# Performance work log

Hardware: AMD Instinct MI355X
Metric: run time of the kernel (lower is better)

The kernel has to match this reference:

```python
import jax, jax.numpy as jnp
import numpy as np

N_NODES = 100000
N_EDGES = 1600000
D_IN = 128
D_OUT = 128
EPSILON = 0.0


def setup_inputs() -> dict:
    key = jax.random.key(0)
    k1, k2, k3, k4, k5 = jax.random.split(key, 5)
    indices = jax.random.randint(k1, (2, N_EDGES), 0, N_NODES, dtype=jnp.int64 if jax.config.jax_enable_x64 else jnp.int32)
    values = jax.random.uniform(k2, (N_EDGES,), dtype=jnp.float32)
    features = jax.random.normal(k3, (N_NODES, D_IN), dtype=jnp.float32)
    # Xavier-uniform linear weights, zero biases (as in init_parameters)
    lim1 = float(np.sqrt(6.0 / (D_IN + D_OUT)))
    lim2 = float(np.sqrt(6.0 / (D_OUT + D_OUT)))
    W1 = jax.random.uniform(k4, (D_IN, D_OUT), minval=-lim1, maxval=lim1, dtype=jnp.float32)
    W2 = jax.random.uniform(k5, (D_OUT, D_OUT), minval=-lim2, maxval=lim2, dtype=jnp.float32)
    b1 = jnp.zeros((D_OUT,), dtype=jnp.float32)
    b2 = jnp.zeros((D_OUT,), dtype=jnp.float32)
    return {"indices": indices, "values": values, "features": features,
            "W1": W1, "b1": b1, "W2": W2, "b2": b2}


def reference(indices, values, features, W1, b1, W2, b2):
    row, col = indices[0], indices[1]
    # SpMM: out[r] = sum_e values[e] * features[col[e]]  (sparse_adj @ features)
    messages = values[:, None] * features[col]              # [E, D_IN]
    neighbor = jax.ops.segment_sum(messages, row, num_segments=N_NODES)  # [N, D_IN]
    combined = (1.0 + EPSILON) * features + neighbor        # epsilon residual
    h = jax.nn.relu(combined @ W1 + b1)                     # Linear -> ReLU
    out = h @ W2 + b2                                       # Linear
    # dropout is identity in eval mode
    return out
```

## Files before the change

kernel.cpp:

```cpp
#include <hip/hip_runtime.h>

#define N_NODES 100000
#define N_EDGES 1600000
#define D 128
#define CB 98
#define CCAP 17920

typedef unsigned short u16;
typedef unsigned int u32;
typedef __attribute__((ext_vector_type(8))) short bf16x8;
typedef __attribute__((ext_vector_type(4))) float f32x4;

__device__ __forceinline__ u16 f2bf(float f) {
    u32 u = __float_as_uint(f);
    u += 0x7fffu + ((u >> 16) & 1u);
    return (u16)(u >> 16);
}


#define BIN_BLKS 391

__global__ __launch_bounds__(256) void prep_bin(
    const int* __restrict__ row, const int* __restrict__ col,
    const float* __restrict__ val,
    int* __restrict__ coarseCount, int2* __restrict__ binned) {
    __shared__ int h[CB];
    __shared__ int lb[CB];
    int bid = blockIdx.x;
    int t = threadIdx.x;

    if (t < CB) h[t] = 0;
    __syncthreads();
    int base = bid * 4096;
    int r[16];
#pragma unroll
    for (int i = 0; i < 16; ++i) {
        int e = base + i * 256 + t;
        r[i] = (e < N_EDGES) ? row[e] : -1;
        if (r[i] >= 0) atomicAdd(&h[r[i] >> 10], 1);
    }
    __syncthreads();
    if (t < CB) {
        int c = h[t];
        lb[t] = c ? atomicAdd(&coarseCount[t * 16], c) : 0;
        h[t] = 0;
    }
    __syncthreads();
#pragma unroll
    for (int i = 0; i < 16; ++i) {
        if (r[i] < 0) continue;
        int e = base + i * 256 + t;
        int cb = r[i] >> 10;
        int pos = cb * CCAP + lb[cb] + atomicAdd(&h[cb], 1);
        int2 ev;
        ev.x = col[e] | ((r[i] & 1023) << 17);
        ev.y = __float_as_int(val[e]);
        binned[pos] = ev;
    }
}


#define SORT_BLKS 98
#define CVF_BLKS 1563
#define CVW_BLKS 32

__global__ __launch_bounds__(1024) void sortk_conv(
    const int2* __restrict__ binned, const int* __restrict__ coarseCount,
    int2* __restrict__ rowRange, int2* __restrict__ scev,
    const float* __restrict__ features, u32* __restrict__ featb,
    const float* __restrict__ W1, const float* __restrict__ W2,
    u16* __restrict__ W1t, u16* __restrict__ W2t) {
    __shared__ int h[1024];
    __shared__ int cur[1024];
    __shared__ int wsum[16];
    __shared__ int wbase[16];
    int b = blockIdx.x, t = threadIdx.x;

    if (b >= SORT_BLKS) {
        int cid = b - SORT_BLKS;
        if (cid < CVF_BLKS) {
            int idx = cid * 1024 + t;
            if (idx < N_NODES * D / 8) {
                const float4* f4 = (const float4*)features;
                float4 a = f4[idx * 2], bb = f4[idx * 2 + 1];
                uint4 o;
                o.x = (u32)f2bf(a.x) | ((u32)f2bf(a.y) << 16);
                o.y = (u32)f2bf(a.z) | ((u32)f2bf(a.w) << 16);
                o.z = (u32)f2bf(bb.x) | ((u32)f2bf(bb.y) << 16);
                o.w = (u32)f2bf(bb.z) | ((u32)f2bf(bb.w) << 16);
                ((uint4*)featb)[idx] = o;
            }
        } else {
            int flat = (cid - CVF_BLKS) * 1024 + t;
            int m = flat >> 14;
            int idx = flat & 16383;
            int n = idx & 127;
            int k = idx >> 7;
            const float* src = m ? W2 : W1;
            u16* dst = m ? W2t : W1t;
            dst[n * 128 + k] = f2bf(src[k * 128 + n]);
        }
        return;
    }

    int lane = t & 63, wv = t >> 6;
    int row0 = b << 10;
    int lo = b * CCAP;
    int cnt = coarseCount[b * 16];

    h[t] = 0;
    __syncthreads();
    for (int i = t; i < cnt; i += 1024)
        atomicAdd(&h[((u32)binned[lo + i].x) >> 17], 1);
    __syncthreads();

    int c = h[t];
    int x = c;
#pragma unroll
    for (int d = 1; d < 64; d <<= 1) {
        int y = __shfl_up(x, d);
        if (lane >= d) x += y;
    }
    if (lane == 63) wsum[wv] = x;
    __syncthreads();
    if (t < 16) {
        int s = wsum[t], sx = s;
#pragma unroll
        for (int d = 1; d < 16; d <<= 1) {
            int y = __shfl_up(sx, d);
            if (lane >= d) sx += y;
        }
        wbase[t] = sx - s;
    }
    __syncthreads();
    int start = lo + wbase[wv] + (x - c);
    if (row0 + t < N_NODES) rowRange[row0 + t] = make_int2(start, start + c);
    cur[t] = start;
    __syncthreads();

    for (int i = t; i < cnt; i += 1024) {
        int2 ev = binned[lo + i];
        int rl = ((u32)ev.x) >> 17;
        int pos = atomicAdd(&cur[rl], 1);
        scev[pos] = make_int2(ev.x & 0x1FFFF, ev.y);
    }
}


__global__ __launch_bounds__(256) void spmm_bf16(
    const int2* __restrict__ scev, const int2* __restrict__ rowRange,
    const u32* __restrict__ featb, u32* __restrict__ Xb) {
    int wid0 = (blockIdx.x * blockDim.x + threadIdx.x) >> 6;
    int wid = __builtin_amdgcn_readfirstlane(wid0);
    int lane = threadIdx.x & 63;
    if (wid >= N_NODES) return;
    int2 rr = rowRange[wid];
    int j = rr.x, end = rr.y;
    u32 self = featb[wid * 64 + lane];
    float ax0 = __uint_as_float(self << 16);
    float ay0 = __uint_as_float(self & 0xffff0000u);
    float ax1 = 0.f, ay1 = 0.f;
    for (; j < end; j += 16) {
        int2 e[16];
        u32 p[16];
#pragma unroll
        for (int u = 0; u < 16; ++u) {
            int idx = j + u;
            int c = (idx < end) ? idx : (end - 1);
            e[u] = scev[c];
            if (idx >= end) e[u].y = 0;
        }
#pragma unroll
        for (int u = 0; u < 16; ++u) p[u] = featb[e[u].x * 64 + lane];
#pragma unroll
        for (int u = 0; u < 16; ++u) {
            float v = __int_as_float(e[u].y);
            float lo = __uint_as_float(p[u] << 16);
            float hi = __uint_as_float(p[u] & 0xffff0000u);
            if (u & 1) {
                ax1 += v * lo;
                ay1 += v * hi;
            } else {
                ax0 += v * lo;
                ay0 += v * hi;
            }
        }
    }
    float accx = ax0 + ax1;
    float accy = ay0 + ay1;
    Xb[wid * 64 + lane] = (u32)f2bf(accx) | ((u32)f2bf(accy) << 16);
}


__global__ __launch_bounds__(256, 2) void gemm_fused(
    const u16* __restrict__ Xb, const u16* __restrict__ W1t,
    const float* __restrict__ b1, const u16* __restrict__ W2t,
    const float* __restrict__ b2, float* __restrict__ outf) {
    __shared__ u16 Ws[128][136];
    u16(*Ht)[130] = (u16(*)[130]) & Ws[0][0];

    int t = threadIdx.x;
    {
        const uint4* wsrc = (const uint4*)W1t;
#pragma unroll
        for (int i = 0; i < 8; ++i) {
            int f = t + 256 * i;
            *(uint4*)&Ws[f >> 4][(f & 15) << 3] = wsrc[f];
        }
    }
    __syncthreads();

    int w = t >> 6, lane = t & 63;
    int quad = lane >> 4, l16 = lane & 15;
    int row0 = blockIdx.x * 128 + w * 32;

    f32x4 acc[2][8];
#pragma unroll
    for (int rt = 0; rt < 2; ++rt)
#pragma unroll
        for (int ct = 0; ct < 8; ++ct) acc[rt][ct] = (f32x4){0.f, 0.f, 0.f, 0.f};

    int ra = row0 + l16;
    int rb = row0 + 16 + l16;
    if (ra > N_NODES - 1) ra = N_NODES - 1;
    if (rb > N_NODES - 1) rb = N_NODES - 1;
    const u16* pa = Xb + (size_t)ra * D + quad * 8;
    const u16* pb = Xb + (size_t)rb * D + quad * 8;

#pragma unroll
    for (int kb = 0; kb < 128; kb += 32) {
        bf16x8 a0 = *(const bf16x8*)(pa + kb);
        bf16x8 a1 = *(const bf16x8*)(pb + kb);
#pragma unroll
        for (int ct = 0; ct < 8; ++ct) {
            bf16x8 b = *(const bf16x8*)&Ws[ct * 16 + l16][kb + quad * 8];
            acc[0][ct] = __builtin_amdgcn_mfma_f32_16x16x32_bf16(a0, b, acc[0][ct], 0, 0, 0);
            acc[1][ct] = __builtin_amdgcn_mfma_f32_16x16x32_bf16(a1, b, acc[1][ct], 0, 0, 0);
        }
    }

    float bv1[8];
#pragma unroll
    for (int ct = 0; ct < 8; ++ct) bv1[ct] = b1[ct * 16 + l16];

    __syncthreads();

    int hbase = w * 32;
#pragma unroll
    for (int rt = 0; rt < 2; ++rt) {
#pragma unroll
        for (int ct = 0; ct < 8; ++ct) {
            float v0 = fmaxf(acc[rt][ct][0] + bv1[ct], 0.f);
            float v1 = fmaxf(acc[rt][ct][1] + bv1[ct], 0.f);
            float v2 = fmaxf(acc[rt][ct][2] + bv1[ct], 0.f);
            float v3 = fmaxf(acc[rt][ct][3] + bv1[ct], 0.f);
            u16* dst = &Ht[ct * 16 + l16][hbase + rt * 16 + quad * 4];
            ((u32*)dst)[0] = (u32)f2bf(v0) | ((u32)f2bf(v1) << 16);
            ((u32*)dst)[1] = (u32)f2bf(v2) | ((u32)f2bf(v3) << 16);
        }
    }
    __syncthreads();

    f32x4 acc2[2][8];
#pragma unroll
    for (int rt = 0; rt < 2; ++rt)
#pragma unroll
        for (int ct = 0; ct < 8; ++ct) acc2[rt][ct] = (f32x4){0.f, 0.f, 0.f, 0.f};

#pragma unroll
    for (int kb = 0; kb < 128; kb += 32) {
        bf16x8 a0, a1;
#pragma unroll
        for (int i = 0; i < 8; ++i) {
            a0[i] = (short)Ht[kb + quad * 8 + i][hbase + l16];
            a1[i] = (short)Ht[kb + quad * 8 + i][hbase + 16 + l16];
        }
#pragma unroll
        for (int ct = 0; ct < 8; ++ct) {
            bf16x8 b = *(const bf16x8*)(W2t + (size_t)(ct * 16 + l16) * D + kb + quad * 8);
            acc2[0][ct] = __builtin_amdgcn_mfma_f32_16x16x32_bf16(a0, b, acc2[0][ct], 0, 0, 0);
            acc2[1][ct] = __builtin_amdgcn_mfma_f32_16x16x32_bf16(a1, b, acc2[1][ct], 0, 0, 0);
        }
    }

    float bv2[8];
#pragma unroll
    for (int ct = 0; ct < 8; ++ct) bv2[ct] = b2[ct * 16 + l16];

#pragma unroll
    for (int rt = 0; rt < 2; ++rt) {
#pragma unroll
        for (int r = 0; r < 4; ++r) {
            int row = row0 + rt * 16 + quad * 4 + r;
            if (row >= N_NODES) continue;
#pragma unroll
            for (int ct = 0; ct < 8; ++ct) {
                outf[(size_t)row * D + ct * 16 + l16] = acc2[rt][ct][r] + bv2[ct];
            }
        }
    }
}

extern "C" void kernel_launch(void* const* d_in, const int* in_sizes, int n_in,
                              void* d_out, int out_size, void* d_ws, size_t ws_size,
                              hipStream_t stream) {
    const int* indices = (const int*)d_in[0];
    const float* values = (const float*)d_in[1];
    const float* features = (const float*)d_in[2];
    const float* W1 = (const float*)d_in[3];
    const float* b1 = (const float*)d_in[4];
    const float* W2 = (const float*)d_in[5];
    const float* b2 = (const float*)d_in[6];

    const int* row = indices;
    const int* col = indices + N_EDGES;

    int* wsI = (int*)d_ws;
    int* coarseCount = wsI;
    int2* rowRange = (int2*)(wsI + 1600);
    int2* scev = (int2*)(wsI + 1600 + 2 * N_NODES);
    u32* Xb = (u32*)(wsI + 1600 + 2 * N_NODES + 2 * CB * CCAP);
    u16* W1t = (u16*)(Xb + (size_t)N_NODES * 64);
    u16* W2t = W1t + 16384;

    int2* binned = (int2*)d_out;
    u32* featb = (u32*)((char*)d_out + (size_t)N_NODES * D * 2);
    float* outf = (float*)d_out;

    hipMemsetAsync(coarseCount, 0, CB * 16 * sizeof(int), stream);

    prep_bin<<<BIN_BLKS, 256, 0, stream>>>(row, col, values, coarseCount, binned);

    sortk_conv<<<SORT_BLKS + CVF_BLKS + CVW_BLKS, 1024, 0, stream>>>(
        binned, coarseCount, rowRange, scev, features, featb, W1, W2, W1t, W2t);

    spmm_bf16<<<(N_NODES * 64 + 255) / 256, 256, 0, stream>>>(scev, rowRange, featb, Xb);

    gemm_fused<<<(N_NODES + 127) / 128, 256, 0, stream>>>(
        (const u16*)Xb, W1t, b1, W2t, b2, outf);
}
```

Before: 254.4 us.

## Halve binning work per block, vectorize SpMM FMAs, raise GEMM occupancy hint

The binning kernel now handles 2048 edges per block instead of 4096 and loads col and val alongside row in the first pass, so they are held in registers and not re-read later. The SpMM accumulation switches to two-wide float vectors so the compiler can emit packed FMA instructions. The fused GEMM launch bound raises its minimum blocks per SM from 2 to 3, which pressures register allocation and risks spills. These are several unrelated tweaks across three kernels.

Result: no change. 254.1 us (-0.1%).

```diff
diff --git a/kernel.cpp b/kernel.cpp
--- a/kernel.cpp
+++ b/kernel.cpp
@@ -10,6 +10,7 @@
 typedef unsigned int u32;
 typedef __attribute__((ext_vector_type(8))) short bf16x8;
 typedef __attribute__((ext_vector_type(4))) float f32x4;
+typedef __attribute__((ext_vector_type(2))) float f32x2;
 
 __device__ __forceinline__ u16 f2bf(float f) {
     u32 u = __float_as_uint(f);
@@ -18,7 +19,7 @@
 }
 
 
-#define BIN_BLKS 391
+#define BIN_BLKS 782
 
 __global__ __launch_bounds__(256) void prep_bin(
     const int* __restrict__ row, const int* __restrict__ col,
@@ -31,30 +32,33 @@
 
     if (t < CB) h[t] = 0;
     __syncthreads();
-    int base = bid * 4096;
-    int r[16];
-#pragma unroll
-    for (int i = 0; i < 16; ++i) {
+    int base = bid * 2048;
+    int r[8], c[8];
+    float v[8];
+#pragma unroll
+    for (int i = 0; i < 8; ++i) {
         int e = base + i * 256 + t;
-        r[i] = (e < N_EDGES) ? row[e] : -1;
-        if (r[i] >= 0) atomicAdd(&h[r[i] >> 10], 1);
+        bool ok = (e < N_EDGES);
+        r[i] = ok ? row[e] : -1;
+        c[i] = ok ? col[e] : 0;
+        v[i] = ok ? val[e] : 0.f;
+        if (ok) atomicAdd(&h[r[i] >> 10], 1);
     }
     __syncthreads();
     if (t < CB) {
-        int c = h[t];
-        lb[t] = c ? atomicAdd(&coarseCount[t * 16], c) : 0;
+        int cc = h[t];
+        lb[t] = cc ? atomicAdd(&coarseCount[t * 16], cc) : 0;
         h[t] = 0;
     }
     __syncthreads();
 #pragma unroll
-    for (int i = 0; i < 16; ++i) {
+    for (int i = 0; i < 8; ++i) {
         if (r[i] < 0) continue;
-        int e = base + i * 256 + t;
         int cb = r[i] >> 10;
         int pos = cb * CCAP + lb[cb] + atomicAdd(&h[cb], 1);
         int2 ev;
-        ev.x = col[e] | ((r[i] & 1023) << 17);
-        ev.y = __float_as_int(val[e]);
+        ev.x = c[i] | ((r[i] & 1023) << 17);
+        ev.y = __float_as_int(v[i]);
         binned[pos] = ev;
     }
 }
@@ -157,9 +161,11 @@
     int2 rr = rowRange[wid];
     int j = rr.x, end = rr.y;
     u32 self = featb[wid * 64 + lane];
-    float ax0 = __uint_as_float(self << 16);
-    float ay0 = __uint_as_float(self & 0xffff0000u);
-    float ax1 = 0.f, ay1 = 0.f;
+    f32x2 acc0, acc1;
+    acc0.x = __uint_as_float(self << 16);
+    acc0.y = __uint_as_float(self & 0xffff0000u);
+    acc1.x = 0.f;
+    acc1.y = 0.f;
     for (; j < end; j += 16) {
         int2 e[16];
         u32 p[16];
@@ -175,24 +181,22 @@
 #pragma unroll
         for (int u = 0; u < 16; ++u) {
             float v = __int_as_float(e[u].y);
-            float lo = __uint_as_float(p[u] << 16);
-            float hi = __uint_as_float(p[u] & 0xffff0000u);
-            if (u & 1) {
-                ax1 += v * lo;
-                ay1 += v * hi;
-            } else {
-                ax0 += v * lo;
-                ay0 += v * hi;
-            }
-        }
-    }
-    float accx = ax0 + ax1;
-    float accy = ay0 + ay1;
+            f32x2 pv, vv;
+            pv.x = __uint_as_float(p[u] << 16);
+            pv.y = __uint_as_float(p[u] & 0xffff0000u);
+            vv.x = v;
+            vv.y = v;
+            if (u & 1) acc1 += vv * pv;
+            else       acc0 += vv * pv;
+        }
+    }
+    float accx = acc0.x + acc1.x;
+    float accy = acc0.y + acc1.y;
     Xb[wid * 64 + lane] = (u32)f2bf(accx) | ((u32)f2bf(accy) << 16);
 }
 
 
-__global__ __launch_bounds__(256, 2) void gemm_fused(
+__global__ __launch_bounds__(256, 3) void gemm_fused(
     const u16* __restrict__ Xb, const u16* __restrict__ W1t,
     const float* __restrict__ b1, const u16* __restrict__ W2t,
     const float* __restrict__ b2, float* __restrict__ outf) {
```
